# Optimization experiments

Hardware: AMD Instinct MI355X
Metric: run time of the kernel (lower is better)

## Reference

```python
import jax, jax.numpy as jnp
import numpy as np

N_ATOMS = 10000
N_PAIR = 100000
F = 128
N_HEAD = 4
FH = F // N_HEAD  # 32
DEGREES = [1, 2, 3]
N_DEG = len(DEGREES)
REPEATS = np.array([2 * l + 1 for l in DEGREES])  # [3,5,7]
M_TOT = int(REPEATS.sum())  # 15
K_RBF = 32


def ssp(x):
    # shifted softplus: softplus(x) - log(2)
    return jax.nn.softplus(x) - jnp.log(2.0).astype(x.dtype)


def setup_inputs() -> dict:
    key = jax.random.key(0)
    ks = jax.random.split(key, 16)
    inp = {
        "x": jax.random.normal(ks[0], (N_ATOMS, F), jnp.float32),
        "rbf_ij": jax.random.normal(ks[1], (N_PAIR, K_RBF), jnp.float32),
        "sph_ij": jax.random.normal(ks[2], (N_PAIR, M_TOT), jnp.float32),
        "phi_r_cut": jax.random.uniform(ks[3], (N_PAIR,), jnp.float32),
        "idx_i": jnp.sort(jax.random.randint(ks[4], (N_PAIR,), 0, N_ATOMS)),
        "idx_j": jax.random.randint(ks[5], (N_PAIR,), 0, N_ATOMS),
        "pair_mask": jnp.ones((N_PAIR,), jnp.float32),
        # params
        "W_Q": jax.random.normal(ks[6], (N_DEG, N_HEAD, FH, FH), jnp.float32) / np.sqrt(FH),
        "W_K": jax.random.normal(ks[7], (N_DEG, N_HEAD, FH, FH), jnp.float32) / np.sqrt(FH),
        # in2f MLP: single dense F -> F
        "W_in": jax.random.normal(ks[8], (F, F), jnp.float32) / np.sqrt(F),
        "b_in": jnp.zeros((F,), jnp.float32),
        # radial filter MLP: K -> K (ssp) -> n_deg*F
        "W_f1": jax.random.normal(ks[9], (K_RBF, K_RBF), jnp.float32) / np.sqrt(K_RBF),
        "b_f1": jnp.zeros((K_RBF,), jnp.float32),
        "W_f2": jax.random.normal(ks[10], (K_RBF, N_DEG * F), jnp.float32) / np.sqrt(K_RBF),
        "b_f2": jnp.zeros((N_DEG * F,), jnp.float32),
        # f2out MLP: single dense F -> F
        "W_out": jax.random.normal(ks[11], (F, F), jnp.float32) / np.sqrt(F),
        "b_out": jnp.zeros((F,), jnp.float32),
    }
    return inp


def reference(x, rbf_ij, sph_ij, phi_r_cut, idx_i, idx_j, pair_mask,
              W_Q, W_K, W_in, b_in, W_f1, b_f1, W_f2, b_f2, W_out, b_out):
    n = x.shape[0]
    # in2f embedding (last in2f dim == F)
    x_f = x @ W_in + b_in                                  # (n, F)
    x_head = x_f.reshape(n, N_HEAD, FH)                    # (n, h, FH)

    # per-degree, per-head linear maps (the nested vmap matmuls)
    Q = jnp.einsum('dhij,nhj->ndhi', W_Q, x_head)          # (n, n_deg, h, FH)
    K = jnp.einsum('dhij,nhj->ndhi', W_K, x_head)

    m = pair_mask[:, None, None, None]
    Q_i = Q[idx_i] * m                                     # (P, n_deg, h, FH)
    K_j = K[idx_j] * m

    # radial filter: MLP(rbf) -> (P, n_deg, h, FH), scaled by cutoff
    h1 = ssp(rbf_ij @ W_f1 + b_f1)
    W_ij = (h1 @ W_f2 + b_f2).reshape(-1, N_DEG, N_HEAD, FH)
    W_ij = W_ij * phi_r_cut[:, None, None, None]

    # attention coefficients per degree/head
    alpha = jnp.sum(Q_i * K_j * W_ij, axis=-1)             # (P, n_deg, h)
    alpha = jnp.repeat(alpha, repeats=REPEATS, axis=1, total_repeat_length=M_TOT)  # (P, m_tot, h)
    alpha = alpha / jnp.sqrt(jnp.asarray(FH, x.dtype))     # att_scale

    # outer product of neighbor features with spherical harmonics
    x_j = x_head[idx_j] * pair_mask[:, None, None]         # (P, h, FH)
    z_ij = jnp.einsum('pm,phf->pmhf', sph_ij, x_j)         # (P, m_tot, h, FH)
    z_ij = alpha[:, :, :, None] * z_ij
    z_ij = z_ij.reshape(z_ij.shape[0], M_TOT, F)           # (P, m_tot, F)

    agg = jax.ops.segment_sum(z_ij, idx_i, num_segments=n)  # (n, m_tot, F)

    # f2out projection (last f2out dim == F)
    out = agg @ W_out + b_out                               # (n, m_tot, F)
    return out
```

## Files before the change

### kernel.cpp

```cpp
#include <hip/hip_runtime.h>
#include <hip/hip_bf16.h>

#define N_ATOMS 10000
#define N_PAIR  100000
#define F_DIM   128
#define N_HEAD  4
#define FH      32
#define N_DEG   3
#define M_TOT   15
#define K_RBF   32

typedef __attribute__((ext_vector_type(8))) short short8;
typedef __attribute__((ext_vector_type(4))) float f32x4;

union frag_cast { int i[4]; short8 s; };

__device__ __forceinline__ float sspf(float v) {
    float sp = fmaxf(v, 0.f) + log1pf(expf(-fabsf(v)));
    return sp - 0.69314718055994531f;
}

__device__ __forceinline__ unsigned short bf16_rne(float x) {
    unsigned int u = __float_as_uint(x);
    unsigned int r = u + 0x7fffu + ((u >> 16) & 1u);
    return (unsigned short)(r >> 16);
}
__device__ __forceinline__ float bf16_tof(unsigned short h) {
    return __uint_as_float(((unsigned int)h) << 16);
}

__global__ __launch_bounds__(256) void k_gemm128(
    const float* __restrict__ A, const float* __restrict__ B,
    const float* __restrict__ bias, float* __restrict__ C, int rows)
{
    __shared__ float As[32][132];
    __shared__ float Bs[32][132];
    int r0 = blockIdx.x * 128;
    int t = threadIdx.x;
    int ty = t >> 4, tx = t & 15;

    float acc[8][8];
    #pragma unroll
    for (int i = 0; i < 8; ++i)
        #pragma unroll
        for (int j = 0; j < 8; ++j) acc[i][j] = 0.f;

    for (int k0 = 0; k0 < 128; k0 += 32) {
        #pragma unroll
        for (int r = 0; r < 16; ++r) {
            int idx = t + 256 * r;
            int row = idx >> 5, kk = idx & 31;
            int grow = r0 + row;
            As[kk][row] = (grow < rows) ? A[grow * 128 + k0 + kk] : 0.f;
        }
        #pragma unroll
        for (int r = 0; r < 16; ++r) {
            int idx = t + 256 * r;
            int kk = idx >> 7, c = idx & 127;
            Bs[kk][c] = B[(k0 + kk) * 128 + c];
        }
        __syncthreads();

        #pragma unroll
        for (int kk = 0; kk < 32; ++kk) {
            float a[8], b[8];
            *(float4*)&a[0] = *(const float4*)&As[kk][ty * 4];
            *(float4*)&a[4] = *(const float4*)&As[kk][64 + ty * 4];
            *(float4*)&b[0] = *(const float4*)&Bs[kk][tx * 4];
            *(float4*)&b[4] = *(const float4*)&Bs[kk][64 + tx * 4];
            #pragma unroll
            for (int i = 0; i < 8; ++i)
                #pragma unroll
                for (int j = 0; j < 8; ++j)
                    acc[i][j] = fmaf(a[i], b[j], acc[i][j]);
        }
        __syncthreads();
    }

    float bj[8];
    #pragma unroll
    for (int j = 0; j < 4; ++j) { bj[j] = bias[tx * 4 + j]; bj[4 + j] = bias[64 + tx * 4 + j]; }

    #pragma unroll
    for (int i = 0; i < 8; ++i) {
        int row = r0 + ((i < 4) ? (ty * 4 + i) : (64 + ty * 4 + (i - 4)));
        if (row < rows) {
            float4 v0, v1;
            v0.x = acc[i][0] + bj[0]; v0.y = acc[i][1] + bj[1];
            v0.z = acc[i][2] + bj[2]; v0.w = acc[i][3] + bj[3];
            v1.x = acc[i][4] + bj[4]; v1.y = acc[i][5] + bj[5];
            v1.z = acc[i][6] + bj[6]; v1.w = acc[i][7] + bj[7];
            *(float4*)&C[row * 128 + tx * 4] = v0;
            *(float4*)&C[row * 128 + 64 + tx * 4] = v1;
        }
    }
}

__global__ __launch_bounds__(384) void k_qk(
    const float* __restrict__ xh, const float* __restrict__ W_Q,
    const float* __restrict__ W_K, float* __restrict__ Q, float* __restrict__ K)
{
    __shared__ float xfs[32][128];
    int t = threadIdx.x;
    int h = (t >> 5) & 3;
    float wq[32], wk[32];
    const float4* wqp = (const float4*)(W_Q + t * 32);
    const float4* wkp = (const float4*)(W_K + t * 32);
    #pragma unroll
    for (int j4 = 0; j4 < 8; ++j4) {
        float4 a = wqp[j4], b = wkp[j4];
        wq[4 * j4 + 0] = a.x; wq[4 * j4 + 1] = a.y; wq[4 * j4 + 2] = a.z; wq[4 * j4 + 3] = a.w;
        wk[4 * j4 + 0] = b.x; wk[4 * j4 + 1] = b.y; wk[4 * j4 + 2] = b.z; wk[4 * j4 + 3] = b.w;
    }
    int ab = blockIdx.x * 32;
    for (int idx = t; idx < 4096; idx += 384) {
        int aa = idx >> 7, f = idx & 127;
        int ag = ab + aa;
        xfs[aa][f] = (ag < N_ATOMS) ? xh[ag * 128 + f] : 0.f;
    }
    __syncthreads();
    for (int aa = 0; aa < 32; ++aa) {
        int ag = ab + aa;
        if (ag >= N_ATOMS) break;
        const float4* xv = (const float4*)&xfs[aa][h * 32];
        float q0 = 0.f, q1 = 0.f, k0 = 0.f, k1 = 0.f;
        #pragma unroll
        for (int j4 = 0; j4 < 8; j4 += 2) {
            float4 x0 = xv[j4], x1 = xv[j4 + 1];
            q0 = fmaf(wq[4 * j4 + 0], x0.x, q0); q0 = fmaf(wq[4 * j4 + 1], x0.y, q0);
            q0 = fmaf(wq[4 * j4 + 2], x0.z, q0); q0 = fmaf(wq[4 * j4 + 3], x0.w, q0);
            q1 = fmaf(wq[4 * j4 + 4], x1.x, q1); q1 = fmaf(wq[4 * j4 + 5], x1.y, q1);
            q1 = fmaf(wq[4 * j4 + 6], x1.z, q1); q1 = fmaf(wq[4 * j4 + 7], x1.w, q1);
            k0 = fmaf(wk[4 * j4 + 0], x0.x, k0); k0 = fmaf(wk[4 * j4 + 1], x0.y, k0);
            k0 = fmaf(wk[4 * j4 + 2], x0.z, k0); k0 = fmaf(wk[4 * j4 + 3], x0.w, k0);
            k1 = fmaf(wk[4 * j4 + 4], x1.x, k1); k1 = fmaf(wk[4 * j4 + 5], x1.y, k1);
            k1 = fmaf(wk[4 * j4 + 6], x1.z, k1); k1 = fmaf(wk[4 * j4 + 7], x1.w, k1);
        }
        Q[ag * 384 + t] = q0 + q1;
        K[ag * 384 + t] = k0 + k1;
    }
}

__global__ __launch_bounds__(256) void k_cvt_w2(
    const float* __restrict__ W, unsigned short* __restrict__ Wh,
    unsigned short* __restrict__ Wl)
{
    int idx = blockIdx.x * 256 + threadIdx.x;
    if (idx < 12288) {
        int e = idx >> 5, k = idx & 31;
        float v = W[k * 384 + e];
        unsigned short h = bf16_rne(v);
        unsigned short l = bf16_rne(v - bf16_tof(h));
        Wh[e * 32 + k] = h;
        Wl[e * 32 + k] = l;
    }
}

__global__ __launch_bounds__(256) void k_pair(
    const float* __restrict__ rbf, const float* __restrict__ phi,
    const float* __restrict__ mask, const int* __restrict__ idx_i,
    const int* __restrict__ idx_j, const float* __restrict__ W_f1,
    const float* __restrict__ b_f1, const unsigned short* __restrict__ W2h,
    const unsigned short* __restrict__ W2l, const float* __restrict__ b_f2,
    const float* __restrict__ Q, const float* __restrict__ K,
    float* __restrict__ alpha)
{
    __shared__ float g_s[16][388];
    __shared__ unsigned int h1p_s[16][36];
    __shared__ int   i_s[16];
    __shared__ int   j_s[16];
    __shared__ float phim_s[16];

    float (*rbf_s)[33] = (float (*)[33])(&g_s[0][0]);
    float (*wf1_s)[33] = (float (*)[33])(&g_s[0][0] + 16 * 33);

    int t = threadIdx.x;
    int p0 = blockIdx.x * 16;

    for (int idx = t; idx < 1536; idx += 256) {
        if (idx < 512) {
            rbf_s[idx >> 5][idx & 31] = rbf[p0 * 32 + idx];
        } else {
            int k = idx - 512;
            wf1_s[k >> 5][k & 31] = W_f1[k];
        }
    }
    if (t < 16) {
        int pg = p0 + t;
        i_s[t] = idx_i[pg];
        j_s[t] = idx_j[pg];
        float m = mask[pg];
        phim_s[t] = phi[pg] * m * m * 0.17677669529663687f;
    }
    __syncthreads();

    {
        int p = t >> 4, c0 = (t & 15) * 2;
        float acc0 = b_f1[c0], acc1 = b_f1[c0 + 1];
        #pragma unroll
        for (int k = 0; k < 32; ++k) {
            float rv = rbf_s[p][k];
            acc0 = fmaf(rv, wf1_s[k][c0], acc0);
            acc1 = fmaf(rv, wf1_s[k][c0 + 1], acc1);
        }
        float h0 = sspf(acc0), h1v = sspf(acc1);
        unsigned short hh0 = bf16_rne(h0);
        unsigned short ll0 = bf16_rne(h0 - bf16_tof(hh0));
        unsigned short hh1 = bf16_rne(h1v);
        unsigned short ll1 = bf16_rne(h1v - bf16_tof(hh1));
        h1p_s[p][c0]     = ((unsigned int)hh0 << 16) | (unsigned int)ll0;
        h1p_s[p][c0 + 1] = ((unsigned int)hh1 << 16) | (unsigned int)ll1;
    }
    __syncthreads();

    #pragma unroll
    for (int it = 0; it < 6; ++it) {
        int idx = it * 256 + t;
        int p = idx / 96;
        int c4 = idx - p * 96;
        const float4* qp = (const float4*)(Q + i_s[p] * 384) + c4;
        const float4* kp = (const float4*)(K + j_s[p] * 384) + c4;
        float4 qv = *qp, kv = *kp;
        float4 gv;
        gv.x = qv.x * kv.x; gv.y = qv.y * kv.y;
        gv.z = qv.z * kv.z; gv.w = qv.w * kv.w;
        *(float4*)&g_s[p][c4 * 4] = gv;
    }
    __syncthreads();

    int wave = t >> 6, lane = t & 63;
    int quad = lane >> 4, l15 = lane & 15;

    short8 ah, al;
    {
        const unsigned int* hp = &h1p_s[l15][quad * 8];
        uint4 u01 = *(const uint4*)hp;
        uint4 u23 = *(const uint4*)(hp + 4);
        unsigned int u[8] = {u01.x, u01.y, u01.z, u01.w, u23.x, u23.y, u23.z, u23.w};
        frag_cast fh, fl;
        #pragma unroll
        for (int q = 0; q < 4; ++q) {
            unsigned int a0 = u[2 * q], a1 = u[2 * q + 1];
            fh.i[q] = (int)((a0 >> 16) | (a1 & 0xffff0000u));
            fl.i[q] = (int)((a0 & 0xffffu) | (a1 << 16));
        }
        ah = fh.s;
        al = fl.s;
    }

    #pragma unroll
    for (int dd = 0; dd < 3; ++dd) {
        int dh = wave * 3 + dd;
        int e_base = dh * 32;
        short8 bh0 = *(const short8*)(W2h + (e_base + l15) * 32 + quad * 8);
        short8 bl0 = *(const short8*)(W2l + (e_base + l15) * 32 + quad * 8);
        short8 bh1 = *(const short8*)(W2h + (e_base + 16 + l15) * 32 + quad * 8);
        short8 bl1 = *(const short8*)(W2l + (e_base + 16 + l15) * 32 + quad * 8);
        float b2v0 = b_f2[e_base + l15];
        float b2v1 = b_f2[e_base + 16 + l15];

        f32x4 s0 = {0.f, 0.f, 0.f, 0.f};
        f32x4 s1 = {0.f, 0.f, 0.f, 0.f};
        s0 = __builtin_amdgcn_mfma_f32_16x16x32_bf16(ah, bh0, s0, 0, 0, 0);
        s1 = __builtin_amdgcn_mfma_f32_16x16x32_bf16(ah, bh1, s1, 0, 0, 0);
        s0 = __builtin_amdgcn_mfma_f32_16x16x32_bf16(al, bh0, s0, 0, 0, 0);
        s1 = __builtin_amdgcn_mfma_f32_16x16x32_bf16(al, bh1, s1, 0, 0, 0);
        s0 = __builtin_amdgcn_mfma_f32_16x16x32_bf16(ah, bl0, s0, 0, 0, 0);
        s1 = __builtin_amdgcn_mfma_f32_16x16x32_bf16(ah, bl1, s1, 0, 0, 0);

        float vsum[4];
        #pragma unroll
        for (int r = 0; r < 4; ++r) {
            int prow = quad * 4 + r;
            float v = (s0[r] + b2v0) * g_s[prow][e_base + l15]
                    + (s1[r] + b2v1) * g_s[prow][e_base + 16 + l15];
            #pragma unroll
            for (int off = 8; off >= 1; off >>= 1)
                v += __shfl_xor(v, off, 16);
            vsum[r] = v;
        }
        if (l15 == 0) {
            #pragma unroll
            for (int r = 0; r < 4; ++r) {
                int prow = quad * 4 + r;
                alpha[(p0 + prow) * 12 + dh] = vsum[r] * phim_s[prow];
            }
        }
    }
}

__device__ __forceinline__ int lower_bound_i(const int* __restrict__ arr, int n, int val) {
    int lo = 0, hi = n;
    while (lo < hi) {
        int mid = (lo + hi) >> 1;
        if (arr[mid] < val) lo = mid + 1; else hi = mid;
    }
    return lo;
}

__global__ __launch_bounds__(256) void k_seg(const int* __restrict__ idx_i,
                                             int* __restrict__ seg)
{
    int a = blockIdx.x * 256 + threadIdx.x;
    if (a <= N_ATOMS) seg[a] = lower_bound_i(idx_i, N_PAIR, a);
}

__global__ __launch_bounds__(256) void k_cvt_b(
    const float* __restrict__ W, unsigned short* __restrict__ Bth,
    unsigned short* __restrict__ Btl)
{
    int idx = blockIdx.x * 256 + threadIdx.x;
    int cc = idx >> 7, kk = idx & 127;
    float v = W[kk * 128 + cc];
    unsigned short h = bf16_rne(v);
    unsigned short l = bf16_rne(v - bf16_tof(h));
    Bth[cc * 128 + kk] = h;
    Btl[cc * 128 + kk] = l;
}

__global__ __launch_bounds__(512) void k_agg_out(
    const float* __restrict__ xh, const float* __restrict__ alpha,
    const float* __restrict__ sph, const int* __restrict__ seg,
    const int* __restrict__ idx_j, const float* __restrict__ mask,
    const unsigned short* __restrict__ Bth, const unsigned short* __restrict__ Btl,
    const float* __restrict__ bias, float* __restrict__ C)
{
    __shared__ float red_s[3][15][132];
    __shared__ unsigned int ap_s[16][132];

    int tid = threadIdx.x;
    int t   = tid & 127;
    int grp = tid >> 7;
    int a = blockIdx.x;
    int h = t >> 5;
    int lo = seg[a], hi = seg[a + 1];

    float acc[15];
    #pragma unroll
    for (int m = 0; m < 15; ++m) acc[m] = 0.f;

    int p = lo + grp;
    float x_c = 0.f, m_c = 0.f, a_c0 = 0.f, a_c1 = 0.f, a_c2 = 0.f;
    float s_c[15];
    int jn = 0;
    if (p < hi) {
        int j0 = idx_j[p];
        m_c  = mask[p];
        a_c0 = alpha[p * 12 + h];
        a_c1 = alpha[p * 12 + 4 + h];
        a_c2 = alpha[p * 12 + 8 + h];
        #pragma unroll
        for (int m = 0; m < 15; ++m) s_c[m] = sph[p * 15 + m];
        x_c = xh[j0 * 128 + t];
        if (p + 4 < hi) jn = idx_j[p + 4];
    }

    while (p < hi) {
        int pn = p + 4;
        float x_n = 0.f, m_n = 0.f, an0 = 0.f, an1 = 0.f, an2 = 0.f;
        float s_n[15];
        #pragma unroll
        for (int m = 0; m < 15; ++m) s_n[m] = 0.f;
        int jn2 = 0;
        if (pn < hi) {
            x_n = xh[jn * 128 + t];
            m_n = mask[pn];
            an0 = alpha[pn * 12 + h];
            an1 = alpha[pn * 12 + 4 + h];
            an2 = alpha[pn * 12 + 8 + h];
            #pragma unroll
            for (int m = 0; m < 15; ++m) s_n[m] = sph[pn * 15 + m];
            if (pn + 4 < hi) jn2 = idx_j[pn + 4];
        }
        float xj = x_c * m_c;
        #pragma unroll
        for (int m = 0; m < 15; ++m) {
            float av = (m < 3) ? a_c0 : ((m < 8) ? a_c1 : a_c2);
            acc[m] = fmaf(s_c[m] * av, xj, acc[m]);
        }
        x_c = x_n; m_c = m_n; a_c0 = an0; a_c1 = an1; a_c2 = an2;
        #pragma unroll
        for (int m = 0; m < 15; ++m) s_c[m] = s_n[m];
        jn = jn2;
        p = pn;
    }

    if (grp >= 1) {
        #pragma unroll
        for (int m = 0; m < 15; ++m) red_s[grp - 1][m][t] = acc[m];
    }
    __syncthreads();
    if (grp == 0) {
        #pragma unroll
        for (int m = 0; m < 15; ++m) {
            float v = acc[m] + red_s[0][m][t] + red_s[1][m][t] + red_s[2][m][t];
            unsigned short hh = bf16_rne(v);
            unsigned short ll = bf16_rne(v - bf16_tof(hh));
            ap_s[m][t] = ((unsigned int)hh << 16) | (unsigned int)ll;
        }
        ap_s[15][t] = 0u;
    }
    __syncthreads();

    int wave = tid >> 6, lane = tid & 63;
    int quad = lane >> 4, l15 = lane & 15;
    int c = wave * 16;

    short8 fa_h[4], fa_l[4];
    #pragma unroll
    for (int ks = 0; ks < 4; ++ks) {
        const unsigned int* hp = &ap_s[l15][ks * 32 + quad * 8];
        uint4 u01 = *(const uint4*)hp;
        uint4 u23 = *(const uint4*)(hp + 4);
        unsigned int u[8] = {u01.x, u01.y, u01.z, u01.w, u23.x, u23.y, u23.z, u23.w};
        frag_cast fh, fl;
        #pragma unroll
        for (int q = 0; q < 4; ++q) {
            unsigned int a0 = u[2 * q], a1 = u[2 * q + 1];
            fh.i[q] = (int)((a0 >> 16) | (a1 & 0xffff0000u));
            fl.i[q] = (int)((a0 & 0xffffu) | (a1 << 16));
        }
        fa_h[ks] = fh.s;
        fa_l[ks] = fl.s;
    }

    short8 bh[4], bl[4];
    #pragma unroll
    for (int ks = 0; ks < 4; ++ks) {
        int off = (c + l15) * 128 + ks * 32 + quad * 8;
        bh[ks] = *(const short8*)(Bth + off);
        bl[ks] = *(const short8*)(Btl + off);
    }
    f32x4 oacc = {0.f, 0.f, 0.f, 0.f};
    #pragma unroll
    for (int ks = 0; ks < 4; ++ks) {
        oacc = __builtin_amdgcn_mfma_f32_16x16x32_bf16(fa_h[ks], bh[ks], oacc, 0, 0, 0);
        oacc = __builtin_amdgcn_mfma_f32_16x16x32_bf16(fa_l[ks], bh[ks], oacc, 0, 0, 0);
        oacc = __builtin_amdgcn_mfma_f32_16x16x32_bf16(fa_h[ks], bl[ks], oacc, 0, 0, 0);
    }
    float bv = bias[c + l15];
    #pragma unroll
    for (int r = 0; r < 4; ++r) {
        int row = quad * 4 + r;
        if (row < 15)
            C[((long)a * 15 + row) * 128 + c + l15] = oacc[r] + bv;
    }
}

extern "C" void kernel_launch(void* const* d_in, const int* in_sizes, int n_in,
                              void* d_out, int out_size, void* d_ws, size_t ws_size,
                              hipStream_t stream) {
    const float* x        = (const float*)d_in[0];
    const float* rbf_ij   = (const float*)d_in[1];
    const float* sph_ij   = (const float*)d_in[2];
    const float* phi_r    = (const float*)d_in[3];
    const int*   idx_i    = (const int*)d_in[4];
    const int*   idx_j    = (const int*)d_in[5];
    const float* pmask    = (const float*)d_in[6];
    const float* W_Q      = (const float*)d_in[7];
    const float* W_K      = (const float*)d_in[8];
    const float* W_in     = (const float*)d_in[9];
    const float* b_in     = (const float*)d_in[10];
    const float* W_f1     = (const float*)d_in[11];
    const float* b_f1     = (const float*)d_in[12];
    const float* W_f2     = (const float*)d_in[13];
    const float* b_f2     = (const float*)d_in[14];
    const float* W_out    = (const float*)d_in[15];
    const float* b_out    = (const float*)d_in[16];
    float* out = (float*)d_out;

    float* ws    = (float*)d_ws;
    float* xh    = ws;
    float* Qbuf  = xh + N_ATOMS * F_DIM;
    float* Kbuf  = Qbuf + N_ATOMS * 384;
    float* alpha = Kbuf + N_ATOMS * 384;
    int*   seg   = (int*)(alpha + N_PAIR * 12);
    unsigned short* Bth = (unsigned short*)(seg + 10432);
    unsigned short* Btl = Bth + 16384;
    unsigned short* W2h = Btl + 16384;
    unsigned short* W2l = W2h + 12288;

    k_seg<<<(N_ATOMS + 256) / 256, 256, 0, stream>>>(idx_i, seg);
    k_cvt_b<<<64, 256, 0, stream>>>(W_out, Bth, Btl);
    k_cvt_w2<<<48, 256, 0, stream>>>(W_f2, W2h, W2l);
    k_gemm128<<<(N_ATOMS + 127) / 128, 256, 0, stream>>>(x, W_in, b_in, xh, N_ATOMS);
    k_qk<<<(N_ATOMS + 31) / 32, 384, 0, stream>>>(xh, W_Q, W_K, Qbuf, Kbuf);
    k_pair<<<N_PAIR / 16, 256, 0, stream>>>(rbf_ij, phi_r, pmask, idx_i, idx_j,
                                            W_f1, b_f1, W2h, W2l, b_f2,
                                            Qbuf, Kbuf, alpha);
    k_agg_out<<<N_ATOMS, 512, 0, stream>>>(xh, alpha, sph_ij, seg, idx_j, pmask,
                                           Bth, Btl, b_out, out);
}
```

Before: 365.8 us.

## Split aggregation into pair-chunked atomic scatter and separate tiled output GEMM

Replaces the per-atom fused aggregate-plus-projection kernel with a kernel that splits pairs into fixed 50-pair chunks. Each chunk accumulates runs of equal idx_i and writes them to the output buffer, using plain stores for atoms wholly inside the chunk and atomics at chunk boundaries. A new kernel then converts the aggregated rows in place to bf16 hi/lo and multiplies them by W_out with MFMA in 64-row tiles, and a zero-fill kernel replaces the segment-offset search. This aims to balance load across uneven neighbour counts and raise MFMA utilisation, at the cost of an extra full round trip of the output through global memory plus atomic traffic.

```diff
diff --git a/kernel.cpp b/kernel.cpp
--- a/kernel.cpp
+++ b/kernel.cpp
@@ -9,6 +9,8 @@
 #define N_DEG   3
 #define M_TOT   15
 #define K_RBF   32
+#define R_OUT   (N_ATOMS * M_TOT)
+#define PPB     50
 
 typedef __attribute__((ext_vector_type(8))) short short8;
 typedef __attribute__((ext_vector_type(4))) float f32x4;
@@ -27,6 +29,14 @@
 }
 __device__ __forceinline__ float bf16_tof(unsigned short h) {
     return __uint_as_float(((unsigned int)h) << 16);
+}
+
+__global__ __launch_bounds__(256) void k_zero(float4* __restrict__ p, int n4)
+{
+    int i = blockIdx.x * 256 + threadIdx.x;
+    int stride = gridDim.x * 256;
+    float4 z = make_float4(0.f, 0.f, 0.f, 0.f);
+    for (; i < n4; i += stride) p[i] = z;
 }
 
 __global__ __launch_bounds__(256) void k_gemm128(
@@ -289,22 +299,6 @@
     }
 }
 
-__device__ __forceinline__ int lower_bound_i(const int* __restrict__ arr, int n, int val) {
-    int lo = 0, hi = n;
-    while (lo < hi) {
-        int mid = (lo + hi) >> 1;
-        if (arr[mid] < val) lo = mid + 1; else hi = mid;
-    }
-    return lo;
-}
-
-__global__ __launch_bounds__(256) void k_seg(const int* __restrict__ idx_i,
-                                             int* __restrict__ seg)
-{
-    int a = blockIdx.x * 256 + threadIdx.x;
-    if (a <= N_ATOMS) seg[a] = lower_bound_i(idx_i, N_PAIR, a);
-}
-
 __global__ __launch_bounds__(256) void k_cvt_b(
     const float* __restrict__ W, unsigned short* __restrict__ Bth,
     unsigned short* __restrict__ Btl)
@@ -318,98 +312,101 @@
     Btl[cc * 128 + kk] = l;
 }
 
-__global__ __launch_bounds__(512) void k_agg_out(
+__device__ __forceinline__ void flush_acc(float* __restrict__ agg, int a,
+                                          const float* acc, int t, bool interior)
+{
+    float* base = agg + (long)a * (M_TOT * 128) + t;
+    if (interior) {
+        #pragma unroll
+        for (int m = 0; m < M_TOT; ++m) base[m * 128] = acc[m];
+    } else {
+        #pragma unroll
+        for (int m = 0; m < M_TOT; ++m) atomicAdd(&base[m * 128], acc[m]);
+    }
+}
+
+__global__ __launch_bounds__(512) void k_aggc(
     const float* __restrict__ xh, const float* __restrict__ alpha,
-    const float* __restrict__ sph, const int* __restrict__ seg,
+    const float* __restrict__ sph, const int* __restrict__ idx_i,
     const int* __restrict__ idx_j, const float* __restrict__ mask,
+    float* __restrict__ agg)
+{
+    int tid = threadIdx.x;
+    int grp = tid >> 7;
+    int t   = tid & 127;
+    int h   = (t >> 5) & 3;
+    int g0  = (blockIdx.x * 4 + grp) * PPB;
+    int g1  = g0 + PPB;
+
+    int prevA = (g0 > 0) ? idx_i[g0 - 1] : -1;
+    int nextA = (g1 < N_PAIR) ? idx_i[g1] : -1;
+
+    float acc[M_TOT];
+    #pragma unroll
+    for (int m = 0; m < M_TOT; ++m) acc[m] = 0.f;
+
+    int cur = idx_i[g0];
+    bool started_inside = (cur != prevA);
+
+    for (int p = g0; p < g1; ++p) {
+        int ii = idx_i[p];
+        if (ii != cur) {
+            flush_acc(agg, cur, acc, t, started_inside);
+            #pragma unroll
+            for (int m = 0; m < M_TOT; ++m) acc[m] = 0.f;
+            cur = ii;
+            started_inside = true;
+        }
+        int jj = idx_j[p];
+        float xj = xh[jj * 128 + t] * mask[p];
+        float a0 = alpha[p * 12 + h];
+        float a1 = alpha[p * 12 + 4 + h];
+        float a2 = alpha[p * 12 + 8 + h];
+        const float* sp = sph + p * 15;
+        #pragma unroll
+        for (int m = 0; m < M_TOT; ++m) {
+            float av = (m < 3) ? a0 : ((m < 8) ? a1 : a2);
+            acc[m] = fmaf(sp[m] * av, xj, acc[m]);
+        }
+    }
+    bool interior = started_inside && (cur != nextA);
+    flush_acc(agg, cur, acc, t, interior);
+}
+
+__global__ __launch_bounds__(256) void k_out2(
     const unsigned short* __restrict__ Bth, const unsigned short* __restrict__ Btl,
     const float* __restrict__ bias, float* __restrict__ C)
 {
-    __shared__ float red_s[3][15][132];
-    __shared__ unsigned int ap_s[16][132];
-
+    __shared__ unsigned int ap_s[64][132];
     int tid = threadIdx.x;
-    int t   = tid & 127;
-    int grp = tid >> 7;
-    int a = blockIdx.x;
-    int h = t >> 5;
-    int lo = seg[a], hi = seg[a + 1];
-
-    float acc[15];
-    #pragma unroll
-    for (int m = 0; m < 15; ++m) acc[m] = 0.f;
-
-    int p = lo + grp;
-    float x_c = 0.f, m_c = 0.f, a_c0 = 0.f, a_c1 = 0.f, a_c2 = 0.f;
-    float s_c[15];
-    int jn = 0;
-    if (p < hi) {
-        int j0 = idx_j[p];
-        m_c  = mask[p];
-        a_c0 = alpha[p * 12 + h];
-        a_c1 = alpha[p * 12 + 4 + h];
-        a_c2 = alpha[p * 12 + 8 + h];
-        #pragma unroll
-        for (int m = 0; m < 15; ++m) s_c[m] = sph[p * 15 + m];
-        x_c = xh[j0 * 128 + t];
-        if (p + 4 < hi) jn = idx_j[p + 4];
-    }
-
-    while (p < hi) {
-        int pn = p + 4;
-        float x_n = 0.f, m_n = 0.f, an0 = 0.f, an1 = 0.f, an2 = 0.f;
-        float s_n[15];
-        #pragma unroll
-        for (int m = 0; m < 15; ++m) s_n[m] = 0.f;
-        int jn2 = 0;
-        if (pn < hi) {
-            x_n = xh[jn * 128 + t];
-            m_n = mask[pn];
-            an0 = alpha[pn * 12 + h];
-            an1 = alpha[pn * 12 + 4 + h];
-            an2 = alpha[pn * 12 + 8 + h];
-            #pragma unroll
-            for (int m = 0; m < 15; ++m) s_n[m] = sph[pn * 15 + m];
-            if (pn + 4 < hi) jn2 = idx_j[pn + 4];
-        }
-        float xj = x_c * m_c;
-        #pragma unroll
-        for (int m = 0; m < 15; ++m) {
-            float av = (m < 3) ? a_c0 : ((m < 8) ? a_c1 : a_c2);
-            acc[m] = fmaf(s_c[m] * av, xj, acc[m]);
-        }
-        x_c = x_n; m_c = m_n; a_c0 = an0; a_c1 = an1; a_c2 = an2;
-        #pragma unroll
-        for (int m = 0; m < 15; ++m) s_c[m] = s_n[m];
-        jn = jn2;
-        p = pn;
-    }
-
-    if (grp >= 1) {
-        #pragma unroll
-        for (int m = 0; m < 15; ++m) red_s[grp - 1][m][t] = acc[m];
-    }
-    __syncthreads();
-    if (grp == 0) {
-        #pragma unroll
-        for (int m = 0; m < 15; ++m) {
-            float v = acc[m] + red_s[0][m][t] + red_s[1][m][t] + red_s[2][m][t];
-            unsigned short hh = bf16_rne(v);
-            unsigned short ll = bf16_rne(v - bf16_tof(hh));
-            ap_s[m][t] = ((unsigned int)hh << 16) | (unsigned int)ll;
-        }
-        ap_s[15][t] = 0u;
+    long r0 = (long)blockIdx.x * 64;
+
+    #pragma unroll
+    for (int it = 0; it < 16; ++it) {
+        int idx = tid + it * 256;
+        int row = idx >> 5, c4 = (idx & 31) * 4;
+        long gr = r0 + row;
+        float4 v = make_float4(0.f, 0.f, 0.f, 0.f);
+        if (gr < (long)R_OUT) v = *(const float4*)(C + gr * 128 + c4);
+        float vv[4] = {v.x, v.y, v.z, v.w};
+        unsigned int pk[4];
+        #pragma unroll
+        for (int q = 0; q < 4; ++q) {
+            unsigned short hh = bf16_rne(vv[q]);
+            unsigned short ll = bf16_rne(vv[q] - bf16_tof(hh));
+            pk[q] = ((unsigned int)hh << 16) | (unsigned int)ll;
+        }
+        *(uint4*)&ap_s[row][c4] = make_uint4(pk[0], pk[1], pk[2], pk[3]);
     }
     __syncthreads();
 
     int wave = tid >> 6, lane = tid & 63;
     int quad = lane >> 4, l15 = lane & 15;
-    int c = wave * 16;
 
     short8 fa_h[4], fa_l[4];
     #pragma unroll
     for (int ks = 0; ks < 4; ++ks) {
-        const unsigned int* hp = &ap_s[l15][ks * 32 + quad * 8];
+        const unsigned int* hp = &ap_s[wave * 16 + l15][ks * 32 + quad * 8];
         uint4 u01 = *(const uint4*)hp;
         uint4 u23 = *(const uint4*)(hp + 4);
         unsigned int u[8] = {u01.x, u01.y, u01.z, u01.w, u23.x, u23.y, u23.z, u23.w};
@@ -424,26 +421,30 @@
         fa_l[ks] = fl.s;
     }
 
-    short8 bh[4], bl[4];
-    #pragma unroll
-    for (int ks = 0; ks < 4; ++ks) {
-        int off = (c + l15) * 128 + ks * 32 + quad * 8;
-        bh[ks] = *(const short8*)(Bth + off);
-        bl[ks] = *(const short8*)(Btl + off);
-    }
-    f32x4 oacc = {0.f, 0.f, 0.f, 0.f};
-    #pragma unroll
-    for (int ks = 0; ks < 4; ++ks) {
-        oacc = __builtin_amdgcn_mfma_f32_16x16x32_bf16(fa_h[ks], bh[ks], oacc, 0, 0, 0);
-        oacc = __builtin_amdgcn_mfma_f32_16x16x32_bf16(fa_l[ks], bh[ks], oacc, 0, 0, 0);
-        oacc = __builtin_amdgcn_mfma_f32_16x16x32_bf16(fa_h[ks], bl[ks], oacc, 0, 0, 0);
-    }
-    float bv = bias[c + l15];
-    #pragma unroll
-    for (int r = 0; r < 4; ++r) {
-        int row = quad * 4 + r;
-        if (row < 15)
-            C[((long)a * 15 + row) * 128 + c + l15] = oacc[r] + bv;
+    #pragma unroll
+    for (int ct = 0; ct < 8; ++ct) {
+        int colbase = ct * 16;
+        short8 bh[4], bl[4];
+        #pragma unroll
+        for (int ks = 0; ks < 4; ++ks) {
+            int off = (colbase + l15) * 128 + ks * 32 + quad * 8;
+            bh[ks] = *(const short8*)(Bth + off);
+            bl[ks] = *(const short8*)(Btl + off);
+        }
+        f32x4 oacc = {0.f, 0.f, 0.f, 0.f};
+        #pragma unroll
+        for (int ks = 0; ks < 4; ++ks) {
+            oacc = __builtin_amdgcn_mfma_f32_16x16x32_bf16(fa_h[ks], bh[ks], oacc, 0, 0, 0);
+            oacc = __builtin_amdgcn_mfma_f32_16x16x32_bf16(fa_l[ks], bh[ks], oacc, 0, 0, 0);
+            oacc = __builtin_amdgcn_mfma_f32_16x16x32_bf16(fa_h[ks], bl[ks], oacc, 0, 0, 0);
+        }
+        float bv = bias[colbase + l15];
+        #pragma unroll
+        for (int r = 0; r < 4; ++r) {
+            long row = r0 + wave * 16 + quad * 4 + r;
+            if (row < (long)R_OUT)
+                C[row * 128 + colbase + l15] = oacc[r] + bv;
+        }
     }
 }
 
@@ -474,13 +475,12 @@
     float* Qbuf  = xh + N_ATOMS * F_DIM;
     float* Kbuf  = Qbuf + N_ATOMS * 384;
     float* alpha = Kbuf + N_ATOMS * 384;
-    int*   seg   = (int*)(alpha + N_PAIR * 12);
-    unsigned short* Bth = (unsigned short*)(seg + 10432);
+    unsigned short* Bth = (unsigned short*)(alpha + N_PAIR * 12);
     unsigned short* Btl = Bth + 16384;
     unsigned short* W2h = Btl + 16384;
     unsigned short* W2l = W2h + 12288;
 
-    k_seg<<<(N_ATOMS + 256) / 256, 256, 0, stream>>>(idx_i, seg);
+    k_zero<<<2048, 256, 0, stream>>>((float4*)d_out, R_OUT * 128 / 4);
     k_cvt_b<<<64, 256, 0, stream>>>(W_out, Bth, Btl);
     k_cvt_w2<<<48, 256, 0, stream>>>(W_f2, W2h, W2l);
     k_gemm128<<<(N_ATOMS + 127) / 128, 256, 0, stream>>>(x, W_in, b_in, xh, N_ATOMS);
@@ -488,6 +488,7 @@
     k_pair<<<N_PAIR / 16, 256, 0, stream>>>(rbf_ij, phi_r, pmask, idx_i, idx_j,
                                             W_f1, b_f1, W2h, W2l, b_f2,
                                             Qbuf, Kbuf, alpha);
-    k_agg_out<<<N_ATOMS, 512, 0, stream>>>(xh, alpha, sph_ij, seg, idx_j, pmask,
-                                           Bth, Btl, b_out, out);
-}
+    k_aggc<<<N_PAIR / (4 * PPB), 512, 0, stream>>>(xh, alpha, sph_ij, idx_i, idx_j,
+                                                   pmask, out);
+    k_out2<<<(R_OUT + 63) / 64, 256, 0, stream>>>(Bth, Btl, b_out, out);
+}
```

New measurement: 440.0 us. 20.3% more time.
